# Kernel tuning notes

Hardware: AMD Instinct MI355X
Metric: run time of the kernel (lower is better)

## Reference

```python
import jax, jax.numpy as jnp
from jax import lax
import numpy as np

NEG = -1e30  # safe log-space -inf for fp32 (avoids inf-inf NaNs)
EPS = 1e-7   # keras.backend.epsilon()


def setup_inputs() -> dict:
    key = jax.random.key(0)
    k1, k2 = jax.random.split(key)
    B, T, C, L = 512, 512, 96, 64
    y_true = jax.random.randint(k1, (B, L), 0, C - 1, dtype=jnp.int64)  # labels in [0, C-2]
    # y_pred mimics softmax output: positive, rows sum to 1
    logits = jax.random.uniform(k2, (B, T, C), dtype=jnp.float32)
    y_pred = logits / jnp.sum(logits, axis=-1, keepdims=True)
    return {"y_true": y_true, "y_pred": y_pred}


def _ctc_batch_cost(y_true, y_pred):
    # Faithful to keras.backend.ctc_batch_cost with full input/label lengths
    # and blank index = num_classes - 1.
    B, T, C = y_pred.shape
    L = y_true.shape[1]
    blank = C - 1
    S = 2 * L + 1  # extended label length: blanks interleaved

    logp = jnp.log(y_pred + EPS)  # [B, T, C]

    # extended label sequence: blank, l0, blank, l1, ..., blank
    ext = jnp.full((B, S), blank, dtype=y_true.dtype).at[:, 1::2].set(y_true)  # [B, S]

    # log-probs of extended labels at every time step: [T, B, S]
    lp = jnp.take_along_axis(
        logp, jnp.broadcast_to(ext[:, None, :], (B, T, S)), axis=2
    ).transpose(1, 0, 2)

    # skip transition (s-2 -> s) allowed iff ext[s] != blank and ext[s] != ext[s-2]
    skip = jnp.concatenate(
        [jnp.zeros((B, 2), dtype=bool),
         (ext[:, 2:] != blank) & (ext[:, 2:] != ext[:, :-2])],
        axis=1,
    )  # [B, S]

    # init: alpha_0(0) = logp(blank), alpha_0(1) = logp(l0)
    alpha0 = jnp.full((B, S), NEG, dtype=logp.dtype)
    alpha0 = alpha0.at[:, 0].set(lp[0, :, 0]).at[:, 1].set(lp[0, :, 1])

    def step(alpha, lp_t):
        s1 = jnp.pad(alpha[:, :-1], ((0, 0), (1, 0)), constant_values=NEG)
        s2 = jnp.pad(alpha[:, :-2], ((0, 0), (2, 0)), constant_values=NEG)
        a = jnp.logaddexp(alpha, s1)
        a = jnp.where(skip, jnp.logaddexp(a, s2), a)
        return a + lp_t, None

    alpha, _ = lax.scan(step, alpha0, lp[1:])
    loss = -jnp.logaddexp(alpha[:, -1], alpha[:, -2])  # [B]
    return loss[:, None]  # [B, 1], matching ctc_batch_cost


def reference(y_true, y_pred):
    return _ctc_batch_cost(y_true, y_pred)
```

## Files before the change

kernel.cpp:

```cpp
#include <hip/hip_runtime.h>
#include <math.h>


constexpr int Bv = 512;
constexpr int Tv = 512;
constexpr int Cv = 96;
constexpr int Lv = 64;
constexpr int BLANK = Cv - 1;
constexpr float EPSf = 1e-7f;

constexpr int ROWS = 32;
constexpr int NCH  = Tv / ROWS;
constexpr int CF   = ROWS * Cv;
constexpr int RS   = 100;
constexpr int SLOTF = ROWS * RS;
constexpr int NSLOT = 4;

__device__ __forceinline__ float dpp_shr1(float x) {
    return __int_as_float(
        __builtin_amdgcn_update_dpp(0, __float_as_int(x), 0x138, 0xf, 0xf, true));
}
template <int C>
__device__ __forceinline__ float dppmax(float m) {
    return fmaxf(m, __int_as_float(
        __builtin_amdgcn_update_dpp(0, __float_as_int(m), C, 0xf, 0xf, true)));
}

__global__ void __launch_bounds__(256, 2) ctc_fwd(const int* __restrict__ y_true,
                                                  const float* __restrict__ y_pred,
                                                  float* __restrict__ out) {
    __shared__ float ring[NSLOT * SLOTF];
    __shared__ int   flags[8];

    const int b = blockIdx.x;
    const int w = threadIdx.x >> 6;
    const int l = threadIdx.x & 63;
    const float* __restrict__ yp = y_pred + (size_t)b * (Tv * Cv);

    if (threadIdx.x < 8) flags[threadIdx.x] = 0;
    __syncthreads();

    if (w != 0) {
#define WA(i) ((((i)*64 + l) / 24) * (RS * 4) + (((i)*64 + l) % 24) * 16)
        const int wa0 = WA(0),  wa1 = WA(1),  wa2 = WA(2),  wa3 = WA(3);
        const int wa4 = WA(4),  wa5 = WA(5),  wa6 = WA(6),  wa7 = WA(7);
        const int wa8 = WA(8),  wa9 = WA(9), wa10 = WA(10), wa11 = WA(11);
#undef WA
        float4 G0,G1,G2,G3,G4,G5,G6,G7,G8,G9,G10,G11;
#define GLOAD(g) do { const float* gp_ = (g) + l * 4;                        \
    G0 = *(const float4*)(gp_ +    0); G1 = *(const float4*)(gp_ +  256);    \
    G2 = *(const float4*)(gp_ +  512); G3 = *(const float4*)(gp_ +  768);    \
    G4 = *(const float4*)(gp_ + 1024); G5 = *(const float4*)(gp_ + 1280);    \
    G6 = *(const float4*)(gp_ + 1536); G7 = *(const float4*)(gp_ + 1792);    \
    G8 = *(const float4*)(gp_ + 2048); G9 = *(const float4*)(gp_ + 2304);    \
    G10= *(const float4*)(gp_ + 2560); G11= *(const float4*)(gp_ + 2816);    \
    } while (0)
#define SWRITE(base) do { char* p_ = (char*)(base);                          \
    *(float4*)(p_ + wa0) = G0;  *(float4*)(p_ + wa1) = G1;                   \
    *(float4*)(p_ + wa2) = G2;  *(float4*)(p_ + wa3) = G3;                   \
    *(float4*)(p_ + wa4) = G4;  *(float4*)(p_ + wa5) = G5;                   \
    *(float4*)(p_ + wa6) = G6;  *(float4*)(p_ + wa7) = G7;                   \
    *(float4*)(p_ + wa8) = G8;  *(float4*)(p_ + wa9) = G9;                   \
    *(float4*)(p_ + wa10)= G10; *(float4*)(p_ + wa11)= G11; } while (0)

        volatile int* cd = &flags[4];
        int c = w - 1;
        GLOAD(yp + (size_t)c * CF);
        while (c < NCH) {
            while (*cd < c - (NSLOT - 1)) __builtin_amdgcn_s_sleep(8);
            SWRITE((char*)ring + (size_t)(c & (NSLOT - 1)) * (SLOTF * 4));
            __builtin_amdgcn_s_waitcnt(0xC07F);
            __asm__ __volatile__("" ::: "memory");
            if (l == 0) *((volatile int*)&flags[c & (NSLOT - 1)]) = c + 1;
            c += 3;
            if (c < NCH) GLOAD(yp + (size_t)c * CF);
        }
#undef GLOAD
#undef SWRITE
        return;
    }

    const int lab   = y_true[b * Lv + l];
    const int labm1 = __shfl_up(lab, 1);
    const bool skip = (l > 0) && (lab != labm1);
    const bool lane0 = (l == 0);

    float a0, a1, a2;
    int   e_acc = 0;
    float sc_p = 1.0f; int e_p = 0;

    auto step = [&](float PB, float PL) {
        float pb  = PB + EPSf;
        float pl  = PL + EPSf;
        float a1p = dpp_shr1(a1);
        float na0 = (a0 + a1p) * pb;
        float s1  = a0 + a1 + (skip ? a1p : 0.0f);
        float na1 = s1 * pl;
        float na2 = (a2 + a1) * pb;
        a0 = na0; a1 = na1; a2 = na2;
    };
    auto rn_apply = [&]() { a0 *= sc_p; a1 *= sc_p; a2 *= sc_p; e_acc += e_p; };
    auto rn_compute = [&]() {
        float m = fmaxf(fmaxf(a0, a1), a2);
        m = dppmax<0x111>(m); m = dppmax<0x112>(m); m = dppmax<0x114>(m);
        m = dppmax<0x118>(m); m = dppmax<0x142>(m); m = dppmax<0x143>(m);
        float mw = __int_as_float(__builtin_amdgcn_readlane(__float_as_int(m), 63));
        unsigned ef = __float_as_uint(mw) >> 23;
        e_p  = (int)ef - 126;
        sc_p = __uint_as_float((253u - ef) << 23);
    };

    float PB0,PB1,PB2,PB3,PB4,PB5,PB6,PB7, PL0,PL1,PL2,PL3,PL4,PL5,PL6,PL7;
    float QB0,QB1,QB2,QB3,QB4,QB5,QB6,QB7, QL0,QL1,QL2,QL3,QL4,QL5,QL6,QL7;
#define LOAD8(P, sb, r0) do {                                                \
    const float* pB_ = (sb) + (r0) * RS + BLANK;                             \
    const float* pL_ = (sb) + (r0) * RS + lab;                               \
    P##B0 = pB_[0*RS]; P##L0 = pL_[0*RS]; P##B1 = pB_[1*RS]; P##L1 = pL_[1*RS];\
    P##B2 = pB_[2*RS]; P##L2 = pL_[2*RS]; P##B3 = pB_[3*RS]; P##L3 = pL_[3*RS];\
    P##B4 = pB_[4*RS]; P##L4 = pL_[4*RS]; P##B5 = pB_[5*RS]; P##L5 = pL_[5*RS];\
    P##B6 = pB_[6*RS]; P##L6 = pL_[6*RS]; P##B7 = pB_[7*RS]; P##L7 = pL_[7*RS];\
    } while (0)
#define STEP_RL(P, i) do { step(P##B##i, P##L##i);                           \
    P##B##i = rb_[(i) * RS]; P##L##i = rl_[(i) * RS]; } while (0)
#define GROUP_RL(P, sb, r16) do {                                            \
    const float* rb_ = (sb) + (r16) * RS + BLANK;                            \
    const float* rl_ = (sb) + (r16) * RS + lab;                              \
    STEP_RL(P,0); STEP_RL(P,1); STEP_RL(P,2); STEP_RL(P,3); rn_apply();      \
    STEP_RL(P,4); STEP_RL(P,5); STEP_RL(P,6); STEP_RL(P,7); rn_compute();    \
    } while (0)
#define GROUP_N(P) do {                                                      \
    step(P##B0,P##L0); step(P##B1,P##L1); step(P##B2,P##L2); step(P##B3,P##L3);\
    rn_apply();                                                              \
    step(P##B4,P##L4); step(P##B5,P##L5); step(P##B6,P##L6); step(P##B7,P##L7);\
    rn_compute(); } while (0)

    volatile int* vf = flags;

    while (vf[0] != 1) __builtin_amdgcn_s_sleep(8);
    __asm__ __volatile__("" ::: "memory");
    {
        const float* sb = ring;
        LOAD8(P, sb, 0); LOAD8(Q, sb, 8);
        a0 = lane0 ? (PB0 + EPSf) : 0.0f;
        a1 = lane0 ? (PL0 + EPSf) : 0.0f;
        a2 = 0.0f;
        {
            const float* rb_ = sb + 16 * RS + BLANK;
            const float* rl_ = sb + 16 * RS + lab;
            PB0 = rb_[0]; PL0 = rl_[0];
            STEP_RL(P,1); STEP_RL(P,2); STEP_RL(P,3); rn_apply();
            STEP_RL(P,4); STEP_RL(P,5); STEP_RL(P,6); STEP_RL(P,7); rn_compute();
        }
        GROUP_RL(Q, sb, 24);
        GROUP_N(P);
        GROUP_N(Q);
    }
    __asm__ __volatile__("" ::: "memory");
    if (l == 0) *((volatile int*)&flags[4]) = 1;

    for (int c = 1; c < NCH; ++c) {
        while (vf[c & (NSLOT - 1)] != c + 1) __builtin_amdgcn_s_sleep(8);
        __asm__ __volatile__("" ::: "memory");
        const float* sb = ring + (size_t)(c & (NSLOT - 1)) * SLOTF;
        LOAD8(P, sb, 0); LOAD8(Q, sb, 8);
        GROUP_RL(P, sb, 16);
        GROUP_RL(Q, sb, 24);
        GROUP_N(P);
        GROUP_N(Q);
        __asm__ __volatile__("" ::: "memory");
        if (l == 0) *((volatile int*)&flags[4]) = c + 1;
    }

    if (l == 63) {
        float sum = a1 + a2;
        out[b] = -(logf(sum) + (float)e_acc * 0.69314718055994530942f);
    }
#undef LOAD8
#undef STEP_RL
#undef GROUP_RL
#undef GROUP_N
}

extern "C" void kernel_launch(void* const* d_in, const int* in_sizes, int n_in,
                              void* d_out, int out_size, void* d_ws, size_t ws_size,
                              hipStream_t stream) {
    const int*   y_true = (const int*)d_in[0];
    const float* y_pred = (const float*)d_in[1];
    float*       out    = (float*)d_out;
    (void)in_sizes; (void)n_in; (void)out_size; (void)d_ws; (void)ws_size;
    ctc_fwd<<<Bv, 256, 0, stream>>>(y_true, y_pred, out);
}
```

Measured before the change: 153.9 us.

## Double-buffer producer loads, move epsilon add to producers, shorten spin sleeps

Producer waves now keep two register sets of prefetched chunks (G/H), issuing loads two chunks ahead and starting them before the initial barrier. The +EPS addition moves from the serial consumer recurrence to the producer waves before the shared-memory write. The skip select becomes an FMA with a 0/1 mask, and the spin-wait sleep intervals are shortened. The aim is to cut the consumer wave's critical-path instructions and to hide global load latency, at the cost of more producer registers.

```diff
diff --git a/kernel.cpp b/kernel.cpp
--- a/kernel.cpp
+++ b/kernel.cpp
@@ -25,6 +25,9 @@
     return fmaxf(m, __int_as_float(
         __builtin_amdgcn_update_dpp(0, __float_as_int(m), C, 0xf, 0xf, true)));
 }
+__device__ __forceinline__ float4 addeps(float4 v) {
+    v.x += EPSf; v.y += EPSf; v.z += EPSf; v.w += EPSf; return v;
+}
 
 __global__ void __launch_bounds__(256, 2) ctc_fwd(const int* __restrict__ y_true,
                                                   const float* __restrict__ y_pred,
@@ -36,9 +39,6 @@
     const int w = threadIdx.x >> 6;
     const int l = threadIdx.x & 63;
     const float* __restrict__ yp = y_pred + (size_t)b * (Tv * Cv);
-
-    if (threadIdx.x < 8) flags[threadIdx.x] = 0;
-    __syncthreads();
 
     if (w != 0) {
 #define WA(i) ((((i)*64 + l) / 24) * (RS * 4) + (((i)*64 + l) % 24) * 16)
@@ -47,64 +47,85 @@
         const int wa8 = WA(8),  wa9 = WA(9), wa10 = WA(10), wa11 = WA(11);
 #undef WA
         float4 G0,G1,G2,G3,G4,G5,G6,G7,G8,G9,G10,G11;
-#define GLOAD(g) do { const float* gp_ = (g) + l * 4;                        \
-    G0 = *(const float4*)(gp_ +    0); G1 = *(const float4*)(gp_ +  256);    \
-    G2 = *(const float4*)(gp_ +  512); G3 = *(const float4*)(gp_ +  768);    \
-    G4 = *(const float4*)(gp_ + 1024); G5 = *(const float4*)(gp_ + 1280);    \
-    G6 = *(const float4*)(gp_ + 1536); G7 = *(const float4*)(gp_ + 1792);    \
-    G8 = *(const float4*)(gp_ + 2048); G9 = *(const float4*)(gp_ + 2304);    \
-    G10= *(const float4*)(gp_ + 2560); G11= *(const float4*)(gp_ + 2816);    \
+        float4 H0,H1,H2,H3,H4,H5,H6,H7,H8,H9,H10,H11;
+#define GLOAD(S, g) do { const float* gp_ = (g) + l * 4;                     \
+    S##0 = *(const float4*)(gp_ +    0); S##1 = *(const float4*)(gp_ +  256);\
+    S##2 = *(const float4*)(gp_ +  512); S##3 = *(const float4*)(gp_ +  768);\
+    S##4 = *(const float4*)(gp_ + 1024); S##5 = *(const float4*)(gp_ + 1280);\
+    S##6 = *(const float4*)(gp_ + 1536); S##7 = *(const float4*)(gp_ + 1792);\
+    S##8 = *(const float4*)(gp_ + 2048); S##9 = *(const float4*)(gp_ + 2304);\
+    S##10= *(const float4*)(gp_ + 2560); S##11= *(const float4*)(gp_ + 2816);\
     } while (0)
-#define SWRITE(base) do { char* p_ = (char*)(base);                          \
-    *(float4*)(p_ + wa0) = G0;  *(float4*)(p_ + wa1) = G1;                   \
-    *(float4*)(p_ + wa2) = G2;  *(float4*)(p_ + wa3) = G3;                   \
-    *(float4*)(p_ + wa4) = G4;  *(float4*)(p_ + wa5) = G5;                   \
-    *(float4*)(p_ + wa6) = G6;  *(float4*)(p_ + wa7) = G7;                   \
-    *(float4*)(p_ + wa8) = G8;  *(float4*)(p_ + wa9) = G9;                   \
-    *(float4*)(p_ + wa10)= G10; *(float4*)(p_ + wa11)= G11; } while (0)
+#define EPSADD(S) do {                                                       \
+    S##0=addeps(S##0); S##1=addeps(S##1); S##2=addeps(S##2);                 \
+    S##3=addeps(S##3); S##4=addeps(S##4); S##5=addeps(S##5);                 \
+    S##6=addeps(S##6); S##7=addeps(S##7); S##8=addeps(S##8);                 \
+    S##9=addeps(S##9); S##10=addeps(S##10); S##11=addeps(S##11); } while (0)
+#define SWRITE(S, base) do { char* p_ = (char*)(base);                       \
+    *(float4*)(p_ + wa0) = S##0;  *(float4*)(p_ + wa1) = S##1;               \
+    *(float4*)(p_ + wa2) = S##2;  *(float4*)(p_ + wa3) = S##3;               \
+    *(float4*)(p_ + wa4) = S##4;  *(float4*)(p_ + wa5) = S##5;               \
+    *(float4*)(p_ + wa6) = S##6;  *(float4*)(p_ + wa7) = S##7;               \
+    *(float4*)(p_ + wa8) = S##8;  *(float4*)(p_ + wa9) = S##9;               \
+    *(float4*)(p_ + wa10)= S##10; *(float4*)(p_ + wa11)= S##11; } while (0)
+
+        int c = w - 1;
+        GLOAD(G, yp + (size_t)c * CF);
+        if (c + 3 < NCH) GLOAD(H, yp + (size_t)(c + 3) * CF);
+        if (l < 8) flags[l] = 0;
+        __syncthreads();
 
         volatile int* cd = &flags[4];
-        int c = w - 1;
-        GLOAD(yp + (size_t)c * CF);
+        bool useG = true;
         while (c < NCH) {
-            while (*cd < c - (NSLOT - 1)) __builtin_amdgcn_s_sleep(8);
-            SWRITE((char*)ring + (size_t)(c & (NSLOT - 1)) * (SLOTF * 4));
+            while (*cd < c - (NSLOT - 1)) __builtin_amdgcn_s_sleep(2);
+            char* base = (char*)ring + (size_t)(c & (NSLOT - 1)) * (SLOTF * 4);
+            if (useG) { EPSADD(G); SWRITE(G, base); }
+            else      { EPSADD(H); SWRITE(H, base); }
             __builtin_amdgcn_s_waitcnt(0xC07F);
             __asm__ __volatile__("" ::: "memory");
             if (l == 0) *((volatile int*)&flags[c & (NSLOT - 1)]) = c + 1;
-            c += 3;
-            if (c < NCH) GLOAD(yp + (size_t)c * CF);
+            int cn = c + 6;
+            if (cn < NCH) {
+                if (useG) GLOAD(G, yp + (size_t)cn * CF);
+                else      GLOAD(H, yp + (size_t)cn * CF);
+            }
+            useG = !useG; c += 3;
         }
 #undef GLOAD
+#undef EPSADD
 #undef SWRITE
         return;
     }
 
     const int lab   = y_true[b * Lv + l];
     const int labm1 = __shfl_up(lab, 1);
-    const bool skip = (l > 0) && (lab != labm1);
+    const float m   = ((l > 0) && (lab != labm1)) ? 1.0f : 0.0f;
     const bool lane0 = (l == 0);
+    if (threadIdx.x < 8) flags[threadIdx.x] = 0;
+    __syncthreads();
 
     float a0, a1, a2;
     int   e_acc = 0;
     float sc_p = 1.0f; int e_p = 0;
 
     auto step = [&](float PB, float PL) {
-        float pb  = PB + EPSf;
-        float pl  = PL + EPSf;
         float a1p = dpp_shr1(a1);
-        float na0 = (a0 + a1p) * pb;
-        float s1  = a0 + a1 + (skip ? a1p : 0.0f);
-        float na1 = s1 * pl;
-        float na2 = (a2 + a1) * pb;
+        float t0  = a0 + a1p;
+        float na0 = t0 * PB;
+        float t01 = a0 + a1;
+        float u   = fmaf(a1p, m, t01);
+        float na1 = u * PL;
+        float t2  = a2 + a1;
+        float na2 = t2 * PB;
         a0 = na0; a1 = na1; a2 = na2;
     };
     auto rn_apply = [&]() { a0 *= sc_p; a1 *= sc_p; a2 *= sc_p; e_acc += e_p; };
     auto rn_compute = [&]() {
-        float m = fmaxf(fmaxf(a0, a1), a2);
-        m = dppmax<0x111>(m); m = dppmax<0x112>(m); m = dppmax<0x114>(m);
-        m = dppmax<0x118>(m); m = dppmax<0x142>(m); m = dppmax<0x143>(m);
-        float mw = __int_as_float(__builtin_amdgcn_readlane(__float_as_int(m), 63));
+        float mx = fmaxf(fmaxf(a0, a1), a2);
+        mx = dppmax<0x111>(mx); mx = dppmax<0x112>(mx); mx = dppmax<0x114>(mx);
+        mx = dppmax<0x118>(mx); mx = dppmax<0x142>(mx); mx = dppmax<0x143>(mx);
+        float mw = __int_as_float(__builtin_amdgcn_readlane(__float_as_int(mx), 63));
         unsigned ef = __float_as_uint(mw) >> 23;
         e_p  = (int)ef - 126;
         sc_p = __uint_as_float((253u - ef) << 23);
@@ -136,13 +157,13 @@
 
     volatile int* vf = flags;
 
-    while (vf[0] != 1) __builtin_amdgcn_s_sleep(8);
+    while (vf[0] != 1) __builtin_amdgcn_s_sleep(1);
     __asm__ __volatile__("" ::: "memory");
     {
         const float* sb = ring;
         LOAD8(P, sb, 0); LOAD8(Q, sb, 8);
-        a0 = lane0 ? (PB0 + EPSf) : 0.0f;
-        a1 = lane0 ? (PL0 + EPSf) : 0.0f;
+        a0 = lane0 ? PB0 : 0.0f;
+        a1 = lane0 ? PL0 : 0.0f;
         a2 = 0.0f;
         {
             const float* rb_ = sb + 16 * RS + BLANK;
@@ -159,7 +180,7 @@
     if (l == 0) *((volatile int*)&flags[4]) = 1;
 
     for (int c = 1; c < NCH; ++c) {
-        while (vf[c & (NSLOT - 1)] != c + 1) __builtin_amdgcn_s_sleep(8);
+        while (vf[c & (NSLOT - 1)] != c + 1) __builtin_amdgcn_s_sleep(1);
         __asm__ __volatile__("" ::: "memory");
         const float* sb = ring + (size_t)(c & (NSLOT - 1)) * SLOTF;
         LOAD8(P, sb, 0); LOAD8(Q, sb, 8);
```

New measurement: 153.4 us. About the same (-0.3%).
